# Optimization experiments

Hardware: AMD Instinct MI355X
Metric: run time of the kernel (lower is better)

The kernel has to match this reference:

```python
import jax, jax.numpy as jnp
import numpy as np

NEG_INF = -1e30


def setup_inputs() -> dict:
    key = jax.random.key(0)
    k1, k2, k3, k4 = jax.random.split(key, 4)
    B, T, C, H = 4, 4096, 1024, 64
    x = jax.random.normal(k1, (B, T, C), dtype=jnp.float32)
    Wk = jax.random.normal(k2, (C, H), dtype=jnp.float32) * (C ** -0.5)
    Wq = jax.random.normal(k3, (C, H), dtype=jnp.float32) * (C ** -0.5)
    Wv = jax.random.normal(k4, (C, H), dtype=jnp.float32) * (C ** -0.5)
    return {"x": x, "Wk": Wk, "Wq": Wq, "Wv": Wv}


def reference(x, Wk, Wq, Wv):
    # x: [B, T, C]; Wq/Wk/Wv: [C, H]
    B, T, C = x.shape
    q = jnp.einsum('btc,ch->bth', x, Wq)  # [B,T,H]
    k = jnp.einsum('btc,ch->bth', x, Wk)  # [B,T,H]
    v = jnp.einsum('btc,ch->bth', x, Wv)  # [B,T,H]
    # NOTE: original scales by C**-0.5 (n_embd), not head_size**-0.5.
    scale = jnp.asarray(C, x.dtype) ** -0.5
    wei = jnp.einsum('bth,bsh->bts', q, k) * scale  # [B,T,T]
    causal = jnp.tril(jnp.ones((T, T), dtype=bool))
    wei = jnp.where(causal, wei, NEG_INF)
    wei = jax.nn.softmax(wei, axis=-1)
    # dropout p=0.0 -> identity
    out = jnp.einsum('bts,bsh->bth', wei, v)  # [B,T,H]
    return out
```

## Files before the change

kernel.cpp:

```cpp
#include <hip/hip_runtime.h>
#include <math.h>

typedef short bfx8 __attribute__((ext_vector_type(8)));
typedef short bfx4 __attribute__((ext_vector_type(4)));
typedef float fx4  __attribute__((ext_vector_type(4)));

__device__ __forceinline__ unsigned short f2bf(float f) {
    unsigned int u = __builtin_bit_cast(unsigned int, f);
    u += 0x7FFFu + ((u >> 16) & 1u);
    return (unsigned short)(u >> 16);
}

__global__ __launch_bounds__(256) void wt_prep(const float* __restrict__ Wq,
                                               const float* __restrict__ Wk,
                                               const float* __restrict__ Wv,
                                               unsigned short* __restrict__ wt)
{
    const int k0  = blockIdx.x * 64;
    const int mat = blockIdx.y;
    const float* W = (mat == 0) ? Wq : ((mat == 1) ? Wk : Wv);
    const float scale = (mat == 0) ? 0.03125f : 1.0f;
    __shared__ unsigned short Ls[64 * 68];
    const int t = threadIdx.x;
    #pragma unroll
    for (int i = 0; i < 4; ++i) {
        int idx4 = t + 256 * i;
        int r = idx4 >> 4, c4 = idx4 & 15;
        float4 v = *(const float4*)&W[(size_t)(k0 + r) * 64 + c4 * 4];
        Ls[r * 68 + c4 * 4 + 0] = f2bf(v.x * scale);
        Ls[r * 68 + c4 * 4 + 1] = f2bf(v.y * scale);
        Ls[r * 68 + c4 * 4 + 2] = f2bf(v.z * scale);
        Ls[r * 68 + c4 * 4 + 3] = f2bf(v.w * scale);
    }
    __syncthreads();
    #pragma unroll
    for (int i = 0; i < 2; ++i) {
        int u = t + 256 * i;
        int n = u >> 3, kc = u & 7;
        bfx8 o;
        #pragma unroll
        for (int j = 0; j < 8; ++j) o[j] = (short)Ls[(kc * 8 + j) * 68 + n];
        *(bfx8*)&wt[(size_t)(mat * 64 + n) * 1024 + k0 + kc * 8] = o;
    }
}

__global__ __launch_bounds__(256) void qkv_mfma(
    const float* __restrict__ x, const unsigned short* __restrict__ wt,
    unsigned short* __restrict__ qb, unsigned short* __restrict__ kb,
    unsigned short* __restrict__ vt)
{
    __shared__ alignas(16) char smem[65536];
    const int t = threadIdx.x;
    const int w = t >> 6, l = t & 63, g = l >> 4, li = l & 15;
    const int m0 = blockIdx.x * 64;

    fx4 acc[12];
    #pragma unroll
    for (int i = 0; i < 12; ++i) acc[i] = (fx4){0.f, 0.f, 0.f, 0.f};

    float4 xr[4]; bfx8 wr[6];

#define QKV_LOAD(K0) do { \
    _Pragma("unroll") for (int i_ = 0; i_ < 4; ++i_) { int idx4 = t + 256 * i_; int r_ = idx4 >> 4, c4 = idx4 & 15; \
        xr[i_] = *(const float4*)&x[(size_t)(m0 + r_) * 1024 + (K0) + c4 * 4]; } \
    _Pragma("unroll") for (int i_ = 0; i_ < 6; ++i_) { int idx = t + 256 * i_; int n_ = idx >> 3, c_ = idx & 7; \
        wr[i_] = *(const bfx8*)&wt[(size_t)n_ * 1024 + (K0) + c_ * 8]; } \
} while (0)

#define QKV_STORE(BI) do { \
    char* xb_ = smem + ((BI) ? 8192 : 0); \
    char* wb_ = smem + 16384 + ((BI) ? 24576 : 0); \
    _Pragma("unroll") for (int i_ = 0; i_ < 4; ++i_) { int idx4 = t + 256 * i_; int r_ = idx4 >> 4, c4 = idx4 & 15; \
        bfx4 o_; o_[0] = (short)f2bf(xr[i_].x); o_[1] = (short)f2bf(xr[i_].y); \
        o_[2] = (short)f2bf(xr[i_].z); o_[3] = (short)f2bf(xr[i_].w); \
        *(bfx4*)(xb_ + ((r_ * 128 + c4 * 8) ^ ((r_ & 7) << 4))) = o_; } \
    _Pragma("unroll") for (int i_ = 0; i_ < 6; ++i_) { int idx = t + 256 * i_; int n_ = idx >> 3, c_ = idx & 7; \
        *(bfx8*)(wb_ + ((n_ * 128 + c_ * 16) ^ ((n_ & 7) << 4))) = wr[i_]; } \
} while (0)

    QKV_LOAD(0); QKV_STORE(0);
    __syncthreads();

    for (int ch = 0; ch < 16; ++ch) {
        if (ch + 1 < 16) QKV_LOAD((ch + 1) * 64);
        if (ch) __syncthreads();
        char* xb = smem + ((ch & 1) ? 8192 : 0);
        char* wb = smem + 16384 + ((ch & 1) ? 24576 : 0);
        const int arow = w * 16 + li;
        #pragma unroll
        for (int kk = 0; kk < 2; ++kk) {
            bfx8 af = *(bfx8*)(xb + ((arow * 128 + kk * 64 + g * 16) ^ ((arow & 7) << 4)));
            #pragma unroll
            for (int nb = 0; nb < 12; ++nb) {
                int nrow = nb * 16 + li;
                bfx8 bf = *(bfx8*)(wb + ((nrow * 128 + kk * 64 + g * 16) ^ ((nrow & 7) << 4)));
                acc[nb] = __builtin_amdgcn_mfma_f32_16x16x32_bf16(af, bf, acc[nb], 0, 0, 0);
            }
        }
        if (ch + 1 < 16) QKV_STORE((ch + 1) & 1);
    }

    const int mrow = m0 + w * 16 + g * 4;
    #pragma unroll
    for (int nb = 0; nb < 4; ++nb)
        #pragma unroll
        for (int r = 0; r < 4; ++r)
            qb[(size_t)(mrow + r) * 64 + nb * 16 + li] = f2bf(acc[nb][r]);
    #pragma unroll
    for (int nb = 4; nb < 8; ++nb)
        #pragma unroll
        for (int r = 0; r < 4; ++r)
            kb[(size_t)(mrow + r) * 64 + (nb - 4) * 16 + li] = f2bf(acc[nb][r]);

    __syncthreads();
    unsigned short* Vt = (unsigned short*)smem;
    #pragma unroll
    for (int nb = 8; nb < 12; ++nb)
        #pragma unroll
        for (int r = 0; r < 4; ++r)
            Vt[((nb - 8) * 16 + li) * 64 + (w * 16 + g * 4 + r)] = f2bf(acc[nb][r]);
    __syncthreads();
    const int bb = m0 >> 12, mt = m0 & 4095;
    #pragma unroll
    for (int i = 0; i < 2; ++i) {
        int idx = t + 256 * i;
        int d = idx >> 3, c = idx & 7;
        *(bfx8*)&vt[((size_t)(bb * 64 + d)) * 4096 + mt + c * 8] = *(bfx8*)&Vt[d * 64 + c * 8];
    }
}

__global__ __launch_bounds__(256) void attn_mfma(
    const unsigned short* __restrict__ qb, const unsigned short* __restrict__ kb,
    const unsigned short* __restrict__ vt, float* __restrict__ out)
{
    __shared__ alignas(16) char smem[69632];
    const int t = threadIdx.x;
    const int w = t >> 6, l = t & 63, g = l >> 4, li = l & 15;
    const int bx = blockIdx.x;
    const int b  = bx & 3;
    const int qt = 127 - (bx >> 2);
    const int qbase = qt * 32;
    const int qsub = w & 1, par = w >> 1;

    const unsigned short* Qg = qb + (size_t)b * 4096 * 64;
    const unsigned short* Kg = kb + (size_t)b * 4096 * 64;
    const unsigned short* Vg = vt + (size_t)b * 64 * 4096;

    const int nch = (qbase + 32 + 127) >> 7;

    bfx8 krg[4], vrg[4];

#define ATT_LOAD(CB) do { \
    _Pragma("unroll") for (int i_ = 0; i_ < 4; ++i_) { int idx = t + 256 * i_; int r_ = idx >> 3, c_ = idx & 7; \
        krg[i_] = *(const bfx8*)&Kg[(size_t)((CB) + r_) * 64 + c_ * 8]; } \
    _Pragma("unroll") for (int i_ = 0; i_ < 4; ++i_) { int idx = t + 256 * i_; int d_ = idx >> 4, c_ = idx & 15; \
        vrg[i_] = *(const bfx8*)&Vg[(size_t)d_ * 4096 + (CB) + c_ * 8]; } \
} while (0)

#define ATT_STORE(BI) do { \
    char* kb_ = smem + 4096 + ((BI) ? 16384 : 0); \
    char* vb_ = smem + 36864 + ((BI) ? 16384 : 0); \
    _Pragma("unroll") for (int i_ = 0; i_ < 4; ++i_) { int idx = t + 256 * i_; int r_ = idx >> 3, c_ = idx & 7; \
        *(bfx8*)(kb_ + ((r_ * 128 + c_ * 16) ^ ((r_ & 7) << 4))) = krg[i_]; } \
    _Pragma("unroll") for (int i_ = 0; i_ < 4; ++i_) { int idx = t + 256 * i_; int d_ = idx >> 4, c_ = idx & 15; \
        *(bfx8*)(vb_ + ((d_ * 256 + c_ * 16) ^ ((d_ & 7) << 4))) = vrg[i_]; } \
} while (0)

    {
        int r2 = t >> 3, c2 = t & 7;
        bfx8 qv = *(const bfx8*)&Qg[(size_t)(qbase + r2) * 64 + c2 * 8];
        *(bfx8*)(smem + ((r2 * 128 + c2 * 16) ^ ((r2 & 7) << 4))) = qv;
    }
    ATT_LOAD(0); ATT_STORE(0);
    __syncthreads();

    const int qrow  = qsub * 16 + li;
    const int qglob = qbase + qrow;
    const bfx8 qf0 = *(bfx8*)(smem + ((qrow * 128 + g * 16)      ^ ((qrow & 7) << 4)));
    const bfx8 qf1 = *(bfx8*)(smem + ((qrow * 128 + 64 + g * 16) ^ ((qrow & 7) << 4)));
    const int qmaxr = qbase + qsub * 16 + 15;

    fx4 o[4];
    #pragma unroll
    for (int i = 0; i < 4; ++i) o[i] = (fx4){0.f, 0.f, 0.f, 0.f};
    float m = -1e30f, lsum = 0.f;

    for (int ch = 0; ch < nch; ++ch) {
        const int cb = ch << 7;
        if (ch + 1 < nch) ATT_LOAD(cb + 128);
        if (ch) __syncthreads();
        char* ks = smem + 4096  + ((ch & 1) ? 16384 : 0);
        char* vs = smem + 36864 + ((ch & 1) ? 16384 : 0);
        const int sub = cb + par * 64;
        if (sub <= qmaxr) {
            fx4 s[4];
            #pragma unroll
            for (int i = 0; i < 4; ++i) s[i] = (fx4){0.f, 0.f, 0.f, 0.f};
            #pragma unroll
            for (int st = 0; st < 4; ++st) {
                int krow = par * 64 + st * 16 + li;
                int sw = (krow & 7) << 4;
                bfx8 kf0 = *(bfx8*)(ks + ((krow * 128 + g * 16)      ^ sw));
                bfx8 kf1 = *(bfx8*)(ks + ((krow * 128 + 64 + g * 16) ^ sw));
                s[st] = __builtin_amdgcn_mfma_f32_16x16x32_bf16(kf0, qf0, s[st], 0, 0, 0);
                s[st] = __builtin_amdgcn_mfma_f32_16x16x32_bf16(kf1, qf1, s[st], 0, 0, 0);
            }
            float p[16]; float pmax = -1e30f;
            #pragma unroll
            for (int st = 0; st < 4; ++st)
                #pragma unroll
                for (int rr = 0; rr < 4; ++rr) {
                    int kv = sub + st * 16 + 4 * g + rr;
                    float vvv = (kv <= qglob) ? s[st][rr] : -1e30f;
                    p[st * 4 + rr] = vvv;
                    pmax = fmaxf(pmax, vvv);
                }
            pmax = fmaxf(pmax, __shfl_xor(pmax, 16));
            pmax = fmaxf(pmax, __shfl_xor(pmax, 32));
            if (__any(pmax > m + 8.f)) {
                float mnew = fmaxf(m, pmax);
                float fac = __expf(m - mnew);
                m = mnew; lsum *= fac;
                #pragma unroll
                for (int d2 = 0; d2 < 4; ++d2) {
                    o[d2][0] *= fac; o[d2][1] *= fac; o[d2][2] *= fac; o[d2][3] *= fac;
                }
            }
            float ps = 0.f;
            #pragma unroll
            for (int e = 0; e < 16; ++e) { p[e] = __expf(p[e] - m); ps += p[e]; }
            ps += __shfl_xor(ps, 16);
            ps += __shfl_xor(ps, 32);
            lsum += ps;
            bfx8 pf0, pf1;
            #pragma unroll
            for (int e = 0; e < 8; ++e) { pf0[e] = (short)f2bf(p[e]); pf1[e] = (short)f2bf(p[8 + e]); }
            #pragma unroll
            for (int dblk = 0; dblk < 4; ++dblk) {
                int dr = dblk * 16 + li;
                int base = dr * 256 + par * 128;
                int sw = (dr & 7) << 4;
                bfx4 a0 = *(bfx4*)(vs + ((base + 8 * g)      ^ sw));
                bfx4 a1 = *(bfx4*)(vs + ((base + 32 + 8 * g) ^ sw));
                bfx8 vf0;
                vf0[0] = a0[0]; vf0[1] = a0[1]; vf0[2] = a0[2]; vf0[3] = a0[3];
                vf0[4] = a1[0]; vf0[5] = a1[1]; vf0[6] = a1[2]; vf0[7] = a1[3];
                o[dblk] = __builtin_amdgcn_mfma_f32_16x16x32_bf16(vf0, pf0, o[dblk], 0, 0, 0);
                bfx4 b0 = *(bfx4*)(vs + ((base + 64 + 8 * g) ^ sw));
                bfx4 b1 = *(bfx4*)(vs + ((base + 96 + 8 * g) ^ sw));
                bfx8 vf1;
                vf1[0] = b0[0]; vf1[1] = b0[1]; vf1[2] = b0[2]; vf1[3] = b0[3];
                vf1[4] = b1[0]; vf1[5] = b1[1]; vf1[6] = b1[2]; vf1[7] = b1[3];
                o[dblk] = __builtin_amdgcn_mfma_f32_16x16x32_bf16(vf1, pf1, o[dblk], 0, 0, 0);
            }
        }
        if (ch + 1 < nch) ATT_STORE((ch + 1) & 1);
    }

    __syncthreads();
    float* Osh = (float*)(smem + 4096);
    float* msh = (float*)smem;
    #pragma unroll
    for (int dblk = 0; dblk < 4; ++dblk)
        #pragma unroll
        for (int r = 0; r < 4; ++r)
            Osh[(w * 16 + li) * 64 + dblk * 16 + g * 4 + r] = o[dblk][r];
    if (g == 0) { msh[w * 16 + li] = m; msh[64 + w * 16 + li] = lsum; }
    __syncthreads();

    const int q = t >> 3, dc = (t & 7) * 8;
    const int ql = q & 15, qs2 = q >> 4;
    const int wA = qs2, wB = qs2 + 2;
    const float mA = msh[wA * 16 + ql], mB = msh[wB * 16 + ql];
    const float lA = msh[64 + wA * 16 + ql], lB = msh[64 + wB * 16 + ql];
    const float M  = fmaxf(mA, mB);
    const float eA = __expf(mA - M), eB = __expf(mB - M);
    const float inv = 1.f / (lA * eA + lB * eB);
    float* orow = out + ((size_t)b * 4096 + qbase + q) * 64 + dc;
    const float* OA = &Osh[(wA * 16 + ql) * 64 + dc];
    const float* OB = &Osh[(wB * 16 + ql) * 64 + dc];
    #pragma unroll
    for (int j = 0; j < 8; ++j)
        orow[j] = (OA[j] * eA + OB[j] * eB) * inv;
}

extern "C" void kernel_launch(void* const* d_in, const int* in_sizes, int n_in,
                              void* d_out, int out_size, void* d_ws, size_t ws_size,
                              hipStream_t stream)
{
    const float* x  = (const float*)d_in[0];
    const float* Wk = (const float*)d_in[1];
    const float* Wq = (const float*)d_in[2];
    const float* Wv = (const float*)d_in[3];
    float* outp = (float*)d_out;

    unsigned short* qbuf = (unsigned short*)d_ws;
    unsigned short* kbuf = qbuf + (1u << 20);
    unsigned short* vtb  = kbuf + (1u << 20);
    unsigned short* wtb  = vtb  + (1u << 20);

    wt_prep<<<dim3(16, 3), 256, 0, stream>>>(Wq, Wk, Wv, wtb);
    qkv_mfma<<<256, 256, 0, stream>>>(x, wtb, qbuf, kbuf, vtb);
    attn_mfma<<<512, 256, 0, stream>>>(qbuf, kbuf, vtb, outp);
}
```

Measured before the change: 70.18 us.

## Split attention KV range into segments with merge kernel, retile QKV and attention

The attention kernel now processes 64-query tiles, each wave covering two 16-row fragments, and splits the causal KV range into 1024-key segments. Each segment writes bf16 partial outputs plus max and sum statistics, and a new merge kernel combines them, which balances work across blocks for long rows. The QKV projection uses 32-row tiles to double its grid size. Softmax switches to exp2 with log2e folded into the Q scale, and MFMA sections get raised scheduling priority. In exchange it adds a fourth launch, workspace traffic for the partials, and bf16 rounding of the partial outputs.

```diff
diff --git a/kernel.cpp b/kernel.cpp
--- a/kernel.cpp
+++ b/kernel.cpp
@@ -9,6 +9,10 @@
     unsigned int u = __builtin_bit_cast(unsigned int, f);
     u += 0x7FFFu + ((u >> 16) & 1u);
     return (unsigned short)(u >> 16);
+}
+__device__ __forceinline__ float bf2f(unsigned short s) {
+    unsigned int u = ((unsigned int)s) << 16;
+    return __builtin_bit_cast(float, u);
 }
 
 __global__ __launch_bounds__(256) void wt_prep(const float* __restrict__ Wq,
@@ -19,7 +23,7 @@
     const int k0  = blockIdx.x * 64;
     const int mat = blockIdx.y;
     const float* W = (mat == 0) ? Wq : ((mat == 1) ? Wk : Wv);
-    const float scale = (mat == 0) ? 0.03125f : 1.0f;
+    const float scale = (mat == 0) ? (0.03125f * 1.4426950408889634f) : 1.0f;
     __shared__ unsigned short Ls[64 * 68];
     const int t = threadIdx.x;
     #pragma unroll
@@ -49,28 +53,30 @@
     unsigned short* __restrict__ qb, unsigned short* __restrict__ kb,
     unsigned short* __restrict__ vt)
 {
-    __shared__ alignas(16) char smem[65536];
+    __shared__ alignas(16) char smem[57344];
     const int t = threadIdx.x;
     const int w = t >> 6, l = t & 63, g = l >> 4, li = l & 15;
-    const int m0 = blockIdx.x * 64;
-
-    fx4 acc[12];
-    #pragma unroll
-    for (int i = 0; i < 12; ++i) acc[i] = (fx4){0.f, 0.f, 0.f, 0.f};
-
-    float4 xr[4]; bfx8 wr[6];
+    const int m0 = blockIdx.x * 32;
+    const int rh  = (w & 1) * 16;
+    const int nb0 = (w >> 1) * 6;
+
+    fx4 acc[6];
+    #pragma unroll
+    for (int i = 0; i < 6; ++i) acc[i] = (fx4){0.f, 0.f, 0.f, 0.f};
+
+    float4 xr[2]; bfx8 wr[6];
 
 #define QKV_LOAD(K0) do { \
-    _Pragma("unroll") for (int i_ = 0; i_ < 4; ++i_) { int idx4 = t + 256 * i_; int r_ = idx4 >> 4, c4 = idx4 & 15; \
+    _Pragma("unroll") for (int i_ = 0; i_ < 2; ++i_) { int idx4 = t + 256 * i_; int r_ = idx4 >> 4, c4 = idx4 & 15; \
         xr[i_] = *(const float4*)&x[(size_t)(m0 + r_) * 1024 + (K0) + c4 * 4]; } \
     _Pragma("unroll") for (int i_ = 0; i_ < 6; ++i_) { int idx = t + 256 * i_; int n_ = idx >> 3, c_ = idx & 7; \
         wr[i_] = *(const bfx8*)&wt[(size_t)n_ * 1024 + (K0) + c_ * 8]; } \
 } while (0)
 
 #define QKV_STORE(BI) do { \
-    char* xb_ = smem + ((BI) ? 8192 : 0); \
-    char* wb_ = smem + 16384 + ((BI) ? 24576 : 0); \
-    _Pragma("unroll") for (int i_ = 0; i_ < 4; ++i_) { int idx4 = t + 256 * i_; int r_ = idx4 >> 4, c4 = idx4 & 15; \
+    char* xb_ = smem + (BI) * 4096; \
+    char* wb_ = smem + 8192 + (BI) * 24576; \
+    _Pragma("unroll") for (int i_ = 0; i_ < 2; ++i_) { int idx4 = t + 256 * i_; int r_ = idx4 >> 4, c4 = idx4 & 15; \
         bfx4 o_; o_[0] = (short)f2bf(xr[i_].x); o_[1] = (short)f2bf(xr[i_].y); \
         o_[2] = (short)f2bf(xr[i_].z); o_[3] = (short)f2bf(xr[i_].w); \
         *(bfx4*)(xb_ + ((r_ * 128 + c4 * 8) ^ ((r_ & 7) << 4))) = o_; } \
@@ -84,15 +90,15 @@
     for (int ch = 0; ch < 16; ++ch) {
         if (ch + 1 < 16) QKV_LOAD((ch + 1) * 64);
         if (ch) __syncthreads();
-        char* xb = smem + ((ch & 1) ? 8192 : 0);
-        char* wb = smem + 16384 + ((ch & 1) ? 24576 : 0);
-        const int arow = w * 16 + li;
+        char* xb = smem + (ch & 1) * 4096;
+        char* wb = smem + 8192 + (ch & 1) * 24576;
+        const int arow = rh + li;
         #pragma unroll
         for (int kk = 0; kk < 2; ++kk) {
             bfx8 af = *(bfx8*)(xb + ((arow * 128 + kk * 64 + g * 16) ^ ((arow & 7) << 4)));
             #pragma unroll
-            for (int nb = 0; nb < 12; ++nb) {
-                int nrow = nb * 16 + li;
+            for (int nb = 0; nb < 6; ++nb) {
+                int nrow = (nb0 + nb) * 16 + li;
                 bfx8 bf = *(bfx8*)(wb + ((nrow * 128 + kk * 64 + g * 16) ^ ((nrow & 7) << 4)));
                 acc[nb] = __builtin_amdgcn_mfma_f32_16x16x32_bf16(af, bf, acc[nb], 0, 0, 0);
             }
@@ -100,53 +106,72 @@
         if (ch + 1 < 16) QKV_STORE((ch + 1) & 1);
     }
 
-    const int mrow = m0 + w * 16 + g * 4;
-    #pragma unroll
-    for (int nb = 0; nb < 4; ++nb)
-        #pragma unroll
-        for (int r = 0; r < 4; ++r)
-            qb[(size_t)(mrow + r) * 64 + nb * 16 + li] = f2bf(acc[nb][r]);
-    #pragma unroll
-    for (int nb = 4; nb < 8; ++nb)
-        #pragma unroll
-        for (int r = 0; r < 4; ++r)
-            kb[(size_t)(mrow + r) * 64 + (nb - 4) * 16 + li] = f2bf(acc[nb][r]);
+    const int mrow = m0 + rh + g * 4;
+    #pragma unroll
+    for (int nb = 0; nb < 6; ++nb) {
+        const int nbg = nb0 + nb;
+        if (nbg < 4) {
+            #pragma unroll
+            for (int r = 0; r < 4; ++r)
+                qb[(size_t)(mrow + r) * 64 + nbg * 16 + li] = f2bf(acc[nb][r]);
+        } else if (nbg < 8) {
+            #pragma unroll
+            for (int r = 0; r < 4; ++r)
+                kb[(size_t)(mrow + r) * 64 + (nbg - 4) * 16 + li] = f2bf(acc[nb][r]);
+        }
+    }
 
     __syncthreads();
     unsigned short* Vt = (unsigned short*)smem;
     #pragma unroll
-    for (int nb = 8; nb < 12; ++nb)
-        #pragma unroll
-        for (int r = 0; r < 4; ++r)
-            Vt[((nb - 8) * 16 + li) * 64 + (w * 16 + g * 4 + r)] = f2bf(acc[nb][r]);
+    for (int nb = 0; nb < 6; ++nb) {
+        const int nbg = nb0 + nb;
+        if (nbg >= 8) {
+            #pragma unroll
+            for (int r = 0; r < 4; ++r)
+                Vt[((nbg - 8) * 16 + li) * 40 + rh + g * 4 + r] = f2bf(acc[nb][r]);
+        }
+    }
     __syncthreads();
     const int bb = m0 >> 12, mt = m0 & 4095;
-    #pragma unroll
-    for (int i = 0; i < 2; ++i) {
-        int idx = t + 256 * i;
-        int d = idx >> 3, c = idx & 7;
-        *(bfx8*)&vt[((size_t)(bb * 64 + d)) * 4096 + mt + c * 8] = *(bfx8*)&Vt[d * 64 + c * 8];
+    {
+        int d = t >> 2, c = t & 3;
+        *(bfx8*)&vt[((size_t)(bb * 64 + d)) * 4096 + mt + c * 8] = *(bfx8*)&Vt[d * 40 + c * 8];
     }
 }
 
 __global__ __launch_bounds__(256) void attn_mfma(
     const unsigned short* __restrict__ qb, const unsigned short* __restrict__ kb,
-    const unsigned short* __restrict__ vt, float* __restrict__ out)
+    const unsigned short* __restrict__ vt,
+    unsigned short* __restrict__ pO, float* __restrict__ pml)
 {
-    __shared__ alignas(16) char smem[69632];
+    __shared__ alignas(16) char smem[73728];
     const int t = threadIdx.x;
     const int w = t >> 6, l = t & 63, g = l >> 4, li = l & 15;
     const int bx = blockIdx.x;
-    const int b  = bx & 3;
-    const int qt = 127 - (bx >> 2);
-    const int qbase = qt * 32;
+
+    int b, qt, seg, kvb, nch;
+    if (bx < 384) {
+        int j = bx >> 2; b = bx & 3;
+        if (j < 48)      { seg = 0; qt = 16 + j; }
+        else if (j < 80) { seg = 1; qt = 32 + (j - 48); }
+        else             { seg = 2; qt = 48 + (j - 80); }
+        kvb = seg * 1024; nch = 8;
+    } else {
+        int j = (bx - 384) >> 2; b = bx & 3;
+        qt = 63 - j; seg = qt >> 4; kvb = seg * 1024;
+        nch = ((qt & 15) + 2) >> 1;
+    }
+    const int qbase = qt * 64;
     const int qsub = w & 1, par = w >> 1;
+    const int qmax_w = qbase + qsub * 32 + 31;
+
+    const int gg = qt >> 4, rr_ = qt & 15;
+    const int slot = b * 160 + (8 * gg * (gg - 1) + rr_ * gg + qt) + seg;
 
     const unsigned short* Qg = qb + (size_t)b * 4096 * 64;
     const unsigned short* Kg = kb + (size_t)b * 4096 * 64;
     const unsigned short* Vg = vt + (size_t)b * 64 * 4096;
-
-    const int nch = (qbase + 32 + 127) >> 7;
 
     bfx8 krg[4], vrg[4];
 
@@ -158,8 +183,8 @@
 } while (0)
 
 #define ATT_STORE(BI) do { \
-    char* kb_ = smem + 4096 + ((BI) ? 16384 : 0); \
-    char* vb_ = smem + 36864 + ((BI) ? 16384 : 0); \
+    char* kb_ = smem + 8192  + (BI) * 16384; \
+    char* vb_ = smem + 40960 + (BI) * 16384; \
     _Pragma("unroll") for (int i_ = 0; i_ < 4; ++i_) { int idx = t + 256 * i_; int r_ = idx >> 3, c_ = idx & 7; \
         *(bfx8*)(kb_ + ((r_ * 128 + c_ * 16) ^ ((r_ & 7) << 4))) = krg[i_]; } \
     _Pragma("unroll") for (int i_ = 0; i_ < 4; ++i_) { int idx = t + 256 * i_; int d_ = idx >> 4, c_ = idx & 15; \
@@ -167,121 +192,230 @@
 } while (0)
 
     {
-        int r2 = t >> 3, c2 = t & 7;
-        bfx8 qv = *(const bfx8*)&Qg[(size_t)(qbase + r2) * 64 + c2 * 8];
-        *(bfx8*)(smem + ((r2 * 128 + c2 * 16) ^ ((r2 & 7) << 4))) = qv;
-    }
-    ATT_LOAD(0); ATT_STORE(0);
-    __syncthreads();
-
-    const int qrow  = qsub * 16 + li;
-    const int qglob = qbase + qrow;
-    const bfx8 qf0 = *(bfx8*)(smem + ((qrow * 128 + g * 16)      ^ ((qrow & 7) << 4)));
-    const bfx8 qf1 = *(bfx8*)(smem + ((qrow * 128 + 64 + g * 16) ^ ((qrow & 7) << 4)));
-    const int qmaxr = qbase + qsub * 16 + 15;
-
-    fx4 o[4];
-    #pragma unroll
-    for (int i = 0; i < 4; ++i) o[i] = (fx4){0.f, 0.f, 0.f, 0.f};
-    float m = -1e30f, lsum = 0.f;
+        #pragma unroll
+        for (int i = 0; i < 2; ++i) {
+            int idx = t + 256 * i;
+            int r2 = idx >> 3, c2 = idx & 7;
+            bfx8 qv = *(const bfx8*)&Qg[(size_t)(qbase + r2) * 64 + c2 * 8];
+            *(bfx8*)(smem + ((r2 * 128 + c2 * 16) ^ ((r2 & 7) << 4))) = qv;
+        }
+    }
+    ATT_LOAD(kvb); ATT_STORE(0);
+    __syncthreads();
+
+    bfx8 qf[2][2];
+    #pragma unroll
+    for (int f = 0; f < 2; ++f) {
+        const int qrow = qsub * 32 + f * 16 + li;
+        const int sw = (qrow & 7) << 4;
+        qf[f][0] = *(bfx8*)(smem + ((qrow * 128 + g * 16) ^ sw));
+        qf[f][1] = *(bfx8*)(smem + ((qrow * 128 + 64 + g * 16) ^ sw));
+    }
+
+    fx4 o[4][2];
+    #pragma unroll
+    for (int i = 0; i < 4; ++i)
+        #pragma unroll
+        for (int f = 0; f < 2; ++f) o[i][f] = (fx4){0.f, 0.f, 0.f, 0.f};
+    float m[2] = {-1e30f, -1e30f}, lsum[2] = {0.f, 0.f};
 
     for (int ch = 0; ch < nch; ++ch) {
-        const int cb = ch << 7;
+        const int cb = kvb + (ch << 7);
         if (ch + 1 < nch) ATT_LOAD(cb + 128);
-        if (ch) __syncthreads();
-        char* ks = smem + 4096  + ((ch & 1) ? 16384 : 0);
-        char* vs = smem + 36864 + ((ch & 1) ? 16384 : 0);
+        char* ks = smem + 8192  + ((ch & 1) ? 16384 : 0);
+        char* vs = smem + 40960 + ((ch & 1) ? 16384 : 0);
         const int sub = cb + par * 64;
-        if (sub <= qmaxr) {
-            fx4 s[4];
-            #pragma unroll
-            for (int i = 0; i < 4; ++i) s[i] = (fx4){0.f, 0.f, 0.f, 0.f};
-            #pragma unroll
-            for (int st = 0; st < 4; ++st) {
-                int krow = par * 64 + st * 16 + li;
-                int sw = (krow & 7) << 4;
-                bfx8 kf0 = *(bfx8*)(ks + ((krow * 128 + g * 16)      ^ sw));
-                bfx8 kf1 = *(bfx8*)(ks + ((krow * 128 + 64 + g * 16) ^ sw));
-                s[st] = __builtin_amdgcn_mfma_f32_16x16x32_bf16(kf0, qf0, s[st], 0, 0, 0);
-                s[st] = __builtin_amdgcn_mfma_f32_16x16x32_bf16(kf1, qf1, s[st], 0, 0, 0);
-            }
-            float p[16]; float pmax = -1e30f;
+        if (sub <= qmax_w) {
+            fx4 s[4][2];
             #pragma unroll
             for (int st = 0; st < 4; ++st)
                 #pragma unroll
-                for (int rr = 0; rr < 4; ++rr) {
-                    int kv = sub + st * 16 + 4 * g + rr;
-                    float vvv = (kv <= qglob) ? s[st][rr] : -1e30f;
-                    p[st * 4 + rr] = vvv;
-                    pmax = fmaxf(pmax, vvv);
-                }
-            pmax = fmaxf(pmax, __shfl_xor(pmax, 16));
-            pmax = fmaxf(pmax, __shfl_xor(pmax, 32));
-            if (__any(pmax > m + 8.f)) {
-                float mnew = fmaxf(m, pmax);
-                float fac = __expf(m - mnew);
-                m = mnew; lsum *= fac;
+                for (int f = 0; f < 2; ++f) s[st][f] = (fx4){0.f, 0.f, 0.f, 0.f};
+            __builtin_amdgcn_s_setprio(1);
+            #pragma unroll
+            for (int st = 0; st < 4; ++st) {
+                const int krow = par * 64 + st * 16 + li;
+                const int sw = (krow & 7) << 4;
+                bfx8 kf0 = *(bfx8*)(ks + ((krow * 128 + g * 16) ^ sw));
+                bfx8 kf1 = *(bfx8*)(ks + ((krow * 128 + 64 + g * 16) ^ sw));
                 #pragma unroll
-                for (int d2 = 0; d2 < 4; ++d2) {
-                    o[d2][0] *= fac; o[d2][1] *= fac; o[d2][2] *= fac; o[d2][3] *= fac;
+                for (int f = 0; f < 2; ++f) {
+                    s[st][f] = __builtin_amdgcn_mfma_f32_16x16x32_bf16(kf0, qf[f][0], s[st][f], 0, 0, 0);
+                    s[st][f] = __builtin_amdgcn_mfma_f32_16x16x32_bf16(kf1, qf[f][1], s[st][f], 0, 0, 0);
                 }
             }
-            float ps = 0.f;
-            #pragma unroll
-            for (int e = 0; e < 16; ++e) { p[e] = __expf(p[e] - m); ps += p[e]; }
-            ps += __shfl_xor(ps, 16);
-            ps += __shfl_xor(ps, 32);
-            lsum += ps;
-            bfx8 pf0, pf1;
-            #pragma unroll
-            for (int e = 0; e < 8; ++e) { pf0[e] = (short)f2bf(p[e]); pf1[e] = (short)f2bf(p[8 + e]); }
+            __builtin_amdgcn_s_setprio(0);
+
+            bfx8 pf0[2], pf1[2];
+            #pragma unroll
+            for (int f = 0; f < 2; ++f) {
+                const int qmin_f = qbase + qsub * 32 + f * 16;
+                float p[16];
+                if (sub + 63 > qmin_f) {
+                    #pragma unroll
+                    for (int st = 0; st < 4; ++st)
+                        #pragma unroll
+                        for (int rr = 0; rr < 4; ++rr) {
+                            int kv = sub + st * 16 + 4 * g + rr;
+                            p[st * 4 + rr] = (kv <= qmin_f + li) ? s[st][f][rr] : -1e30f;
+                        }
+                } else {
+                    #pragma unroll
+                    for (int st = 0; st < 4; ++st)
+                        #pragma unroll
+                        for (int rr = 0; rr < 4; ++rr) p[st * 4 + rr] = s[st][f][rr];
+                }
+                float x0 = fmaxf(fmaxf(p[0], p[1]), fmaxf(p[2], p[3]));
+                float x1 = fmaxf(fmaxf(p[4], p[5]), fmaxf(p[6], p[7]));
+                float x2 = fmaxf(fmaxf(p[8], p[9]), fmaxf(p[10], p[11]));
+                float x3 = fmaxf(fmaxf(p[12], p[13]), fmaxf(p[14], p[15]));
+                float pmax = fmaxf(fmaxf(x0, x1), fmaxf(x2, x3));
+                pmax = fmaxf(pmax, __shfl_xor(pmax, 16));
+                pmax = fmaxf(pmax, __shfl_xor(pmax, 32));
+                if (__any(pmax > m[f] + 8.f)) {
+                    float mnew = fmaxf(m[f], pmax);
+                    float fac = exp2f(m[f] - mnew);
+                    m[f] = mnew; lsum[f] *= fac;
+                    #pragma unroll
+                    for (int d2 = 0; d2 < 4; ++d2) {
+                        o[d2][f][0] *= fac; o[d2][f][1] *= fac;
+                        o[d2][f][2] *= fac; o[d2][f][3] *= fac;
+                    }
+                }
+                #pragma unroll
+                for (int e = 0; e < 16; ++e) p[e] = exp2f(p[e] - m[f]);
+                lsum[f] += (((p[0]+p[1])+(p[2]+p[3])) + ((p[4]+p[5])+(p[6]+p[7])))
+                         + (((p[8]+p[9])+(p[10]+p[11])) + ((p[12]+p[13])+(p[14]+p[15])));
+                #pragma unroll
+                for (int e = 0; e < 8; ++e) {
+                    pf0[f][e] = (short)f2bf(p[e]);
+                    pf1[f][e] = (short)f2bf(p[8 + e]);
+                }
+            }
+
+            __builtin_amdgcn_s_setprio(1);
             #pragma unroll
             for (int dblk = 0; dblk < 4; ++dblk) {
-                int dr = dblk * 16 + li;
-                int base = dr * 256 + par * 128;
-                int sw = (dr & 7) << 4;
+                const int dr = dblk * 16 + li;
+                const int base = dr * 256 + par * 128;
+                const int sw = (dr & 7) << 4;
                 bfx4 a0 = *(bfx4*)(vs + ((base + 8 * g)      ^ sw));
                 bfx4 a1 = *(bfx4*)(vs + ((base + 32 + 8 * g) ^ sw));
                 bfx8 vf0;
                 vf0[0] = a0[0]; vf0[1] = a0[1]; vf0[2] = a0[2]; vf0[3] = a0[3];
                 vf0[4] = a1[0]; vf0[5] = a1[1]; vf0[6] = a1[2]; vf0[7] = a1[3];
-                o[dblk] = __builtin_amdgcn_mfma_f32_16x16x32_bf16(vf0, pf0, o[dblk], 0, 0, 0);
                 bfx4 b0 = *(bfx4*)(vs + ((base + 64 + 8 * g) ^ sw));
                 bfx4 b1 = *(bfx4*)(vs + ((base + 96 + 8 * g) ^ sw));
                 bfx8 vf1;
                 vf1[0] = b0[0]; vf1[1] = b0[1]; vf1[2] = b0[2]; vf1[3] = b0[3];
                 vf1[4] = b1[0]; vf1[5] = b1[1]; vf1[6] = b1[2]; vf1[7] = b1[3];
-                o[dblk] = __builtin_amdgcn_mfma_f32_16x16x32_bf16(vf1, pf1, o[dblk], 0, 0, 0);
+                #pragma unroll
+                for (int f = 0; f < 2; ++f) {
+                    o[dblk][f] = __builtin_amdgcn_mfma_f32_16x16x32_bf16(vf0, pf0[f], o[dblk][f], 0, 0, 0);
+                    o[dblk][f] = __builtin_amdgcn_mfma_f32_16x16x32_bf16(vf1, pf1[f], o[dblk][f], 0, 0, 0);
+                }
             }
+            __builtin_amdgcn_s_setprio(0);
         }
         if (ch + 1 < nch) ATT_STORE((ch + 1) & 1);
-    }
-
-    __syncthreads();
-    float* Osh = (float*)(smem + 4096);
-    float* msh = (float*)smem;
+        __syncthreads();
+    }
+
+    float* Osh = (float*)smem;
+    float* msh = (float*)(smem + 32768);
+    float* lsh = (float*)(smem + 33280);
     #pragma unroll
     for (int dblk = 0; dblk < 4; ++dblk)
         #pragma unroll
-        for (int r = 0; r < 4; ++r)
-            Osh[(w * 16 + li) * 64 + dblk * 16 + g * 4 + r] = o[dblk][r];
-    if (g == 0) { msh[w * 16 + li] = m; msh[64 + w * 16 + li] = lsum; }
-    __syncthreads();
-
-    const int q = t >> 3, dc = (t & 7) * 8;
-    const int ql = q & 15, qs2 = q >> 4;
-    const int wA = qs2, wB = qs2 + 2;
-    const float mA = msh[wA * 16 + ql], mB = msh[wB * 16 + ql];
-    const float lA = msh[64 + wA * 16 + ql], lB = msh[64 + wB * 16 + ql];
-    const float M  = fmaxf(mA, mB);
-    const float eA = __expf(mA - M), eB = __expf(mB - M);
-    const float inv = 1.f / (lA * eA + lB * eB);
-    float* orow = out + ((size_t)b * 4096 + qbase + q) * 64 + dc;
-    const float* OA = &Osh[(wA * 16 + ql) * 64 + dc];
-    const float* OB = &Osh[(wB * 16 + ql) * 64 + dc];
-    #pragma unroll
-    for (int j = 0; j < 8; ++j)
-        orow[j] = (OA[j] * eA + OB[j] * eB) * inv;
+        for (int f = 0; f < 2; ++f)
+            #pragma unroll
+            for (int r = 0; r < 4; ++r)
+                Osh[(w * 32 + f * 16 + li) * 64 + dblk * 16 + g * 4 + r] = o[dblk][f][r];
+    #pragma unroll
+    for (int f = 0; f < 2; ++f) {
+        if (g == 0) msh[(w * 2 + f) * 16 + li] = m[f];
+        lsh[((w * 2 + f) * 4 + g) * 16 + li] = lsum[f];
+    }
+    __syncthreads();
+
+    {
+        const int q = t >> 2, dg = t & 3;
+        const int A = q >> 5, Bw = A + 2, fq = (q >> 4) & 1, liq = q & 15, row32 = q & 31;
+        const float mA = msh[(A * 2 + fq) * 16 + liq];
+        const float mB = msh[(Bw * 2 + fq) * 16 + liq];
+        const float lA = lsh[((A * 2 + fq) * 4 + 0) * 16 + liq] + lsh[((A * 2 + fq) * 4 + 1) * 16 + liq]
+                       + lsh[((A * 2 + fq) * 4 + 2) * 16 + liq] + lsh[((A * 2 + fq) * 4 + 3) * 16 + liq];
+        const float lB = lsh[((Bw * 2 + fq) * 4 + 0) * 16 + liq] + lsh[((Bw * 2 + fq) * 4 + 1) * 16 + liq]
+                       + lsh[((Bw * 2 + fq) * 4 + 2) * 16 + liq] + lsh[((Bw * 2 + fq) * 4 + 3) * 16 + liq];
+        const float M = fmaxf(mA, mB);
+        const float eA = exp2f(mA - M), eB = exp2f(mB - M);
+        const float L = lA * eA + lB * eB;
+        const float* OA = &Osh[(A * 32 + row32) * 64 + dg * 16];
+        const float* OB = &Osh[(Bw * 32 + row32) * 64 + dg * 16];
+        bfx8 o1_, o2_;
+        #pragma unroll
+        for (int j = 0; j < 8; ++j) o1_[j] = (short)f2bf(OA[j] * eA + OB[j] * eB);
+        #pragma unroll
+        for (int j = 0; j < 8; ++j) o2_[j] = (short)f2bf(OA[8 + j] * eA + OB[8 + j] * eB);
+        unsigned short* dst = pO + (size_t)slot * 4096 + q * 64 + dg * 16;
+        *(bfx8*)&dst[0] = o1_;
+        *(bfx8*)&dst[8] = o2_;
+        if (dg == 0) {
+            pml[(size_t)slot * 128 + q] = M;
+            pml[(size_t)slot * 128 + 64 + q] = L;
+        }
+    }
+}
+
+__global__ __launch_bounds__(256) void attn_merge(
+    const unsigned short* __restrict__ pO, const float* __restrict__ pml,
+    float* __restrict__ out)
+{
+    const int b = blockIdx.x & 3, qt = blockIdx.x >> 2;
+    const int gg = qt >> 4, rr = qt & 15;
+    const int nseg = gg + 1;
+    const int slot0 = b * 160 + (8 * gg * (gg - 1) + rr * gg + qt);
+    const int t = threadIdx.x;
+    const int q = t >> 2, dg = t & 3;
+
+    float ms[4];
+    float M = -1e30f;
+    #pragma unroll
+    for (int s = 0; s < 4; ++s) {
+        if (s < nseg) { ms[s] = pml[(size_t)(slot0 + s) * 128 + q]; M = fmaxf(M, ms[s]); }
+    }
+    float L = 0.f, es[4];
+    #pragma unroll
+    for (int s = 0; s < 4; ++s) {
+        if (s < nseg) {
+            es[s] = exp2f(ms[s] - M);
+            L += es[s] * pml[(size_t)(slot0 + s) * 128 + 64 + q];
+        }
+    }
+    float acc[16];
+    #pragma unroll
+    for (int j = 0; j < 16; ++j) acc[j] = 0.f;
+    #pragma unroll
+    for (int s = 0; s < 4; ++s) {
+        if (s < nseg) {
+            const unsigned short* src = pO + (size_t)(slot0 + s) * 4096 + q * 64 + dg * 16;
+            bfx8 v0 = *(const bfx8*)&src[0];
+            bfx8 v1 = *(const bfx8*)&src[8];
+            #pragma unroll
+            for (int j = 0; j < 8; ++j) acc[j]     += bf2f((unsigned short)v0[j]) * es[s];
+            #pragma unroll
+            for (int j = 0; j < 8; ++j) acc[8 + j] += bf2f((unsigned short)v1[j]) * es[s];
+        }
+    }
+    const float inv = 1.f / L;
+    float* orow = out + ((size_t)b * 4096 + qt * 64 + q) * 64 + dg * 16;
+    #pragma unroll
+    for (int v4 = 0; v4 < 4; ++v4) {
+        float4 r;
+        r.x = acc[v4 * 4 + 0] * inv; r.y = acc[v4 * 4 + 1] * inv;
+        r.z = acc[v4 * 4 + 2] * inv; r.w = acc[v4 * 4 + 3] * inv;
+        *(float4*)&orow[v4 * 4] = r;
+    }
 }
 
 extern "C" void kernel_launch(void* const* d_in, const int* in_sizes, int n_in,
@@ -294,12 +428,16 @@
     const float* Wv = (const float*)d_in[3];
     float* outp = (float*)d_out;
 
-    unsigned short* qbuf = (unsigned short*)d_ws;
-    unsigned short* kbuf = qbuf + (1u << 20);
-    unsigned short* vtb  = kbuf + (1u << 20);
-    unsigned short* wtb  = vtb  + (1u << 20);
+    char* ws = (char*)d_ws;
+    unsigned short* qbuf = (unsigned short*)(ws);
+    unsigned short* kbuf = (unsigned short*)(ws + 2*1024*1024);
+    unsigned short* vtb  = (unsigned short*)(ws + 4*1024*1024);
+    unsigned short* wtb  = (unsigned short*)(ws + 6*1024*1024);
+    unsigned short* pO   = (unsigned short*)(ws + 7*1024*1024);
+    float*          pml  = (float*)(ws + 12*1024*1024 + 65536);
 
     wt_prep<<<dim3(16, 3), 256, 0, stream>>>(Wq, Wk, Wv, wtb);
-    qkv_mfma<<<256, 256, 0, stream>>>(x, wtb, qbuf, kbuf, vtb);
-    attn_mfma<<<512, 256, 0, stream>>>(qbuf, kbuf, vtb, outp);
-}
+    qkv_mfma<<<512, 256, 0, stream>>>(x, wtb, qbuf, kbuf, vtb);
+    attn_mfma<<<640, 256, 0, stream>>>(qbuf, kbuf, vtb, pO, pml);
+    attn_merge<<<256, 256, 0, stream>>>(pO, pml, outp);
+}
```

Measured after the change: 74.66 us. +6.4%, slower.
